# Kernel optimization log

Hardware: AMD Instinct MI355X
Metric: run time of the kernel (lower is better)

## Reference

```python
import jax, jax.numpy as jnp
import numpy as np

N_VIEWS = 2
TEMPERATURE = 0.07


def setup_inputs() -> dict:
    key = jax.random.key(0)
    # concatenated features for n_views=2 views of batch_size=4096, proj dim 128
    features = jax.random.normal(key, (8192, 128), dtype=jnp.float32)
    return {"features": features}


def reference(features) -> jnp.ndarray:
    # NT-Xent / SimCLR loss, faithful to the torch module:
    #   sim = F F^T ; drop diagonal ; logits = [positive, negatives] / T ;
    #   CE with label 0  ==  mean( logsumexp(off_diag/T) - positive/T )
    # (concatenating [pos, neg] is a row permutation of the off-diagonal
    #  entries, and CrossEntropy(label=0) only needs logsumexp(row) - pos.)
    N = features.shape[0]
    B = N // N_VIEWS
    inv_t = 1.0 / TEMPERATURE

    sim = jnp.matmul(features, features.T)  # [N, N]

    row = jnp.arange(N)
    # off-diagonal column indices in increasing-j order, matching mask.view:
    # cols[i] = [0..i-1, i+1..N-1]
    cols = jnp.arange(N - 1)[None, :]
    cols = cols + (cols >= row[:, None])  # [N, N-1]
    sim_offdiag = jnp.take_along_axis(sim, cols, axis=1)  # [N, N-1]

    # with n_views=2 the single positive for row i is its other view (i+B) % N
    pos = sim[row, (row + B) % N]  # [N]

    lse = jax.nn.logsumexp(sim_offdiag * inv_t, axis=1)  # [N]
    loss = jnp.mean(lse - pos * inv_t)
    return loss
```

## Files before the change

kernel.cpp:

```cpp
#include <hip/hip_runtime.h>
#include <math.h>

typedef __bf16 bf16x8 __attribute__((ext_vector_type(8)));
typedef float f32x4 __attribute__((ext_vector_type(4)));
typedef unsigned short u16x8 __attribute__((ext_vector_type(8)));

#define N_TOT 8192
#define HALF_N 4096
#define D 128
#define INV_T 14.285714285714286f
#define CSC 20.609929155556627f
#define NCSC -20.609929155556627f
#define LN2F 0.69314718055994531f
#define NEG_BIG -3.0e38f
#define M_INIT -1.0e30f
#define THR_RAW 1.0f
#define CS 16

__device__ __forceinline__ unsigned short f2bf(float f) {
    union { float f; unsigned int u; } a; a.f = f;
    unsigned int u = a.u;
    return (unsigned short)((u + 0x7fffu + ((u >> 16) & 1u)) >> 16);
}

__global__ __launch_bounds__(256)
void cvt_kernel(const float* __restrict__ in, unsigned short* __restrict__ fbP) {
    const int c   = blockIdx.x * 256 + threadIdx.x;
    const int q   = c >> 6;
    const int rem = c & 63;
    const int lg  = rem >> 4, lr = rem & 15;
    const int kk  = q & 3;
    const int col = (q >> 2) * 16 + lr;
    const int j16 = kk * 4 + lg;
    const float4 v0 = reinterpret_cast<const float4*>(in)[col * 32 + j16 * 2];
    const float4 v1 = reinterpret_cast<const float4*>(in)[col * 32 + j16 * 2 + 1];
    u16x8 o;
    o[0] = f2bf(v0.x); o[1] = f2bf(v0.y); o[2] = f2bf(v0.z); o[3] = f2bf(v0.w);
    o[4] = f2bf(v1.x); o[5] = f2bf(v1.y); o[6] = f2bf(v1.z); o[7] = f2bf(v1.w);
    reinterpret_cast<u16x8*>(fbP)[c] = o;
}

__global__ __launch_bounds__(256, 3)
void simclr_kernel(const unsigned short* __restrict__ fbP,
                   float* __restrict__ pm, float* __restrict__ ps,
                   float* __restrict__ rowpos) {
    __shared__ __align__(16) unsigned short lds[2][8192];
    const int tid  = threadIdx.x;
    const int lane = tid & 63;
    const int wid  = tid >> 6;
    const int lr   = lane & 15;
    const int lg   = lane >> 4;
    const int RT0  = blockIdx.x * 16 + wid * 4;
    const int Tw   = blockIdx.y * 32;

    bf16x8 br[4][4];
#pragma unroll
    for (int rt = 0; rt < 4; ++rt)
#pragma unroll
        for (int kk = 0; kk < 4; ++kk)
            br[rt][kk] = *reinterpret_cast<const bf16x8*>(
                fbP + ((size_t)(((RT0 + rt) * 4 + kk) * 64) + lane) * 8);

    float m[4], s[4];
#pragma unroll
    for (int rt = 0; rt < 4; ++rt) { m[rt] = M_INIT; s[rt] = 0.f; }

    auto stage = [&](int q, int b) {
#pragma unroll
        for (int h = 0; h < 4; ++h) {
            const unsigned short* src =
                fbP + ((size_t)(Tw + 4 * q + h) * 256 + tid) * 8;
            unsigned short* dst = &lds[b][(h * 256 + tid) * 8];
            __builtin_amdgcn_global_load_lds(
                (const __attribute__((address_space(1))) unsigned int*)(const void*)src,
                (__attribute__((address_space(3))) unsigned int*)(void*)dst,
                16, 0, 0);
        }
    };

    stage(0, 0);
    __syncthreads();

    int buf = 0;
#pragma unroll 1
    for (int q = 0; q < 8; ++q) {
        if (q < 7) stage(q + 1, buf ^ 1);

#pragma unroll
        for (int pp = 0; pp < 2; ++pp) {
            const unsigned short* B = &lds[buf][pp * 4096];
            bf16x8 ca[4], cb[4];
#pragma unroll
            for (int kk = 0; kk < 4; ++kk) {
                ca[kk] = *reinterpret_cast<const bf16x8*>(&B[(kk * 64 + lane) * 8]);
                cb[kk] = *reinterpret_cast<const bf16x8*>(&B[((kk + 4) * 64 + lane) * 8]);
            }

            const int c0 = blockIdx.y * 512 + (q * 4 + pp * 2) * 16;

            f32x4 accP[4], accQ[4];
#pragma unroll
            for (int rt = 0; rt < 4; ++rt) accP[rt] = f32x4{0.f, 0.f, 0.f, 0.f};
#pragma unroll
            for (int kk = 0; kk < 4; ++kk)
#pragma unroll
                for (int rt = 0; rt < 4; ++rt)
                    accP[rt] = __builtin_amdgcn_mfma_f32_16x16x32_bf16(ca[kk], br[rt][kk], accP[rt], 0, 0, 0);
#pragma unroll
            for (int rt = 0; rt < 4; ++rt) accQ[rt] = f32x4{0.f, 0.f, 0.f, 0.f};
#pragma unroll
            for (int kk = 0; kk < 4; ++kk)
#pragma unroll
                for (int rt = 0; rt < 4; ++rt)
                    accQ[rt] = __builtin_amdgcn_mfma_f32_16x16x32_bf16(cb[kk], br[rt][kk], accQ[rt], 0, 0, 0);

#pragma unroll
            for (int rt = 0; rt < 4; ++rt) {
                const int rowbase = (RT0 + rt) * 16;
                f32x4 P = accP[rt], Q = accQ[rt];
                if (c0 == (rowbase ^ HALF_N)) {
#pragma unroll
                    for (int r = 0; r < 4; ++r)
                        if (lr == lg * 4 + r) rowpos[rowbase + lr] = P[r];
                }
                if (c0 + 16 == (rowbase ^ HALF_N)) {
#pragma unroll
                    for (int r = 0; r < 4; ++r)
                        if (lr == lg * 4 + r) rowpos[rowbase + lr] = Q[r];
                }
                if (c0 == rowbase) {
#pragma unroll
                    for (int r = 0; r < 4; ++r)
                        if (lr == lg * 4 + r) P[r] = NEG_BIG;
                }
                if (c0 + 16 == rowbase) {
#pragma unroll
                    for (int r = 0; r < 4; ++r)
                        if (lr == lg * 4 + r) Q[r] = NEG_BIG;
                }
                const float t1 = fmaxf(fmaxf(P[0], P[1]), P[2]);
                const float t2 = fmaxf(fmaxf(P[3], Q[0]), Q[1]);
                const float t3 = fmaxf(Q[2], Q[3]);
                const float rmax = fmaxf(fmaxf(t1, t2), t3);
                if (!__all(rmax <= m[rt] + THR_RAW)) {
                    const float mn = fmaxf(m[rt], rmax);
                    s[rt] *= __builtin_amdgcn_exp2f(fmaf(m[rt], CSC, mn * NCSC));
                    m[rt] = mn;
                }
                const float cm = m[rt] * NCSC;
                const float e0 = __builtin_amdgcn_exp2f(fmaf(P[0], CSC, cm));
                const float e1 = __builtin_amdgcn_exp2f(fmaf(P[1], CSC, cm));
                const float e2 = __builtin_amdgcn_exp2f(fmaf(P[2], CSC, cm));
                const float e3 = __builtin_amdgcn_exp2f(fmaf(P[3], CSC, cm));
                const float e4 = __builtin_amdgcn_exp2f(fmaf(Q[0], CSC, cm));
                const float e5 = __builtin_amdgcn_exp2f(fmaf(Q[1], CSC, cm));
                const float e6 = __builtin_amdgcn_exp2f(fmaf(Q[2], CSC, cm));
                const float e7 = __builtin_amdgcn_exp2f(fmaf(Q[3], CSC, cm));
                s[rt] += ((e0 + e1) + (e2 + e3)) + ((e4 + e5) + (e6 + e7));
            }
        }

        __syncthreads();
        buf ^= 1;
    }

#pragma unroll
    for (int rt = 0; rt < 4; ++rt) {
        float M = m[rt];
        M = fmaxf(M, __shfl_xor(M, 16, 64));
        M = fmaxf(M, __shfl_xor(M, 32, 64));
        float sc = s[rt] * __builtin_amdgcn_exp2f(fmaf(m[rt], CSC, M * NCSC));
        sc += __shfl_xor(sc, 16, 64);
        sc += __shfl_xor(sc, 32, 64);
        if (lg == 0) {
            const int row = (RT0 + rt) * 16 + lr;
            pm[blockIdx.y * N_TOT + row] = M;
            ps[blockIdx.y * N_TOT + row] = sc;
        }
    }
}

__global__ __launch_bounds__(256)
void rowloss_mean_kernel(const float* __restrict__ pm, const float* __restrict__ ps,
                         const float* __restrict__ rowpos, float* __restrict__ out) {
    const int row = blockIdx.x * 256 + threadIdx.x;
    float M = pm[row], S = ps[row];
#pragma unroll
    for (int c = 1; c < CS; ++c) {
        const float Mo = pm[c * N_TOT + row], So = ps[c * N_TOT + row];
        const float mn = fmaxf(M, Mo);
        S = fmaf(S,  __builtin_amdgcn_exp2f(fmaf(M,  CSC, mn * NCSC)),
                 So * __builtin_amdgcn_exp2f(fmaf(Mo, CSC, mn * NCSC)));
        M = mn;
    }
    float acc = LN2F * fmaf(M, CSC, __builtin_amdgcn_logf(S)) - rowpos[row] * INV_T;
#pragma unroll
    for (int off = 32; off > 0; off >>= 1) acc += __shfl_xor(acc, off, 64);
    __shared__ float ls[4];
    if ((threadIdx.x & 63) == 0) ls[threadIdx.x >> 6] = acc;
    __syncthreads();
    if (threadIdx.x == 0)
        atomicAdd(out, (ls[0] + ls[1] + ls[2] + ls[3]) * (1.0f / (float)N_TOT));
}

extern "C" void kernel_launch(void* const* d_in, const int* in_sizes, int n_in,
                              void* d_out, int out_size, void* d_ws, size_t ws_size,
                              hipStream_t stream) {
    const float* feat = (const float*)d_in[0];
    char* ws = (char*)d_ws;
    unsigned short* fbP = (unsigned short*)ws;
    float* pm      = (float*)(ws + (size_t)N_TOT * D * 2);
    float* ps      = (float*)(ws + (size_t)N_TOT * D * 2 + (size_t)CS * N_TOT * 4);
    float* rowpos  = (float*)(ws + (size_t)N_TOT * D * 2 + 2 * (size_t)CS * N_TOT * 4);
    float* out = (float*)d_out;

    hipMemsetAsync(out, 0, sizeof(float), stream);
    cvt_kernel<<<512, 256, 0, stream>>>(feat, fbP);
    simclr_kernel<<<dim3(32, CS), 256, 0, stream>>>(fbP, pm, ps, rowpos);
    rowloss_mean_kernel<<<N_TOT / 256, 256, 0, stream>>>(pm, ps, rowpos, out);
}
```

Baseline: 40.49 us.

## Use single barrier per tile and compute positive dot in final kernel

Result: slower. 47.77 us (+18.0%).

```diff
diff --git a/kernel.cpp b/kernel.cpp
--- a/kernel.cpp
+++ b/kernel.cpp
@@ -40,10 +40,9 @@
     reinterpret_cast<u16x8*>(fbP)[c] = o;
 }
 
-__global__ __launch_bounds__(256, 3)
+__global__ __launch_bounds__(256)
 void simclr_kernel(const unsigned short* __restrict__ fbP,
-                   float* __restrict__ pm, float* __restrict__ ps,
-                   float* __restrict__ rowpos) {
+                   float* __restrict__ pm, float* __restrict__ ps) {
     __shared__ __align__(16) unsigned short lds[2][8192];
     const int tid  = threadIdx.x;
     const int lane = tid & 63;
@@ -79,12 +78,15 @@
     };
 
     stage(0, 0);
-    __syncthreads();
 
     int buf = 0;
 #pragma unroll 1
     for (int q = 0; q < 8; ++q) {
-        if (q < 7) stage(q + 1, buf ^ 1);
+        __builtin_amdgcn_sched_barrier(0);
+        asm volatile("s_waitcnt vmcnt(0)" ::: "memory");
+        __builtin_amdgcn_s_barrier();
+        asm volatile("" ::: "memory");
+        __builtin_amdgcn_sched_barrier(0);
 
 #pragma unroll
         for (int pp = 0; pp < 2; ++pp) {
@@ -95,6 +97,7 @@
                 ca[kk] = *reinterpret_cast<const bf16x8*>(&B[(kk * 64 + lane) * 8]);
                 cb[kk] = *reinterpret_cast<const bf16x8*>(&B[((kk + 4) * 64 + lane) * 8]);
             }
+            if (pp == 0 && q < 7) stage(q + 1, buf ^ 1);
 
             const int c0 = blockIdx.y * 512 + (q * 4 + pp * 2) * 16;
 
@@ -118,16 +121,6 @@
             for (int rt = 0; rt < 4; ++rt) {
                 const int rowbase = (RT0 + rt) * 16;
                 f32x4 P = accP[rt], Q = accQ[rt];
-                if (c0 == (rowbase ^ HALF_N)) {
-#pragma unroll
-                    for (int r = 0; r < 4; ++r)
-                        if (lr == lg * 4 + r) rowpos[rowbase + lr] = P[r];
-                }
-                if (c0 + 16 == (rowbase ^ HALF_N)) {
-#pragma unroll
-                    for (int r = 0; r < 4; ++r)
-                        if (lr == lg * 4 + r) rowpos[rowbase + lr] = Q[r];
-                }
                 if (c0 == rowbase) {
 #pragma unroll
                     for (int r = 0; r < 4; ++r)
@@ -159,8 +152,6 @@
                 s[rt] += ((e0 + e1) + (e2 + e3)) + ((e4 + e5) + (e6 + e7));
             }
         }
-
-        __syncthreads();
         buf ^= 1;
     }
 
@@ -182,7 +173,7 @@
 
 __global__ __launch_bounds__(256)
 void rowloss_mean_kernel(const float* __restrict__ pm, const float* __restrict__ ps,
-                         const float* __restrict__ rowpos, float* __restrict__ out) {
+                         const float* __restrict__ feat, float* __restrict__ out) {
     const int row = blockIdx.x * 256 + threadIdx.x;
     float M = pm[row], S = ps[row];
 #pragma unroll
@@ -193,7 +184,15 @@
                  So * __builtin_amdgcn_exp2f(fmaf(Mo, CSC, mn * NCSC)));
         M = mn;
     }
-    float acc = LN2F * fmaf(M, CSC, __builtin_amdgcn_logf(S)) - rowpos[row] * INV_T;
+    const float4* f = reinterpret_cast<const float4*>(feat + (size_t)row * D);
+    const float4* g = reinterpret_cast<const float4*>(feat + (size_t)(row ^ HALF_N) * D);
+    float dot = 0.f;
+#pragma unroll
+    for (int j = 0; j < 32; ++j) {
+        const float4 a = f[j], b = g[j];
+        dot += a.x * b.x + a.y * b.y + a.z * b.z + a.w * b.w;
+    }
+    float acc = LN2F * fmaf(M, CSC, __builtin_amdgcn_logf(S)) - dot * INV_T;
 #pragma unroll
     for (int off = 32; off > 0; off >>= 1) acc += __shfl_xor(acc, off, 64);
     __shared__ float ls[4];
@@ -211,11 +210,10 @@
     unsigned short* fbP = (unsigned short*)ws;
     float* pm      = (float*)(ws + (size_t)N_TOT * D * 2);
     float* ps      = (float*)(ws + (size_t)N_TOT * D * 2 + (size_t)CS * N_TOT * 4);
-    float* rowpos  = (float*)(ws + (size_t)N_TOT * D * 2 + 2 * (size_t)CS * N_TOT * 4);
     float* out = (float*)d_out;
 
     hipMemsetAsync(out, 0, sizeof(float), stream);
     cvt_kernel<<<512, 256, 0, stream>>>(feat, fbP);
-    simclr_kernel<<<dim3(32, CS), 256, 0, stream>>>(fbP, pm, ps, rowpos);
-    rowloss_mean_kernel<<<N_TOT / 256, 256, 0, stream>>>(pm, ps, rowpos, out);
-}
+    simclr_kernel<<<dim3(32, CS), 256, 0, stream>>>(fbP, pm, ps);
+    rowloss_mean_kernel<<<N_TOT / 256, 256, 0, stream>>>(pm, ps, feat, out);
+}
```
